# Kernel optimization log

Hardware: AMD Instinct MI355X
Metric: run time of the kernel (lower is better)

Reference implementation:

```python
import jax, jax.numpy as jnp
import numpy as np

B, S, H, G, W = 4, 4096, 1024, 256, 8
CHUNK = 1024
NUM_HEADS = 4


def _ln(x, g, b, eps=1e-5):
    m = jnp.mean(x, axis=-1, keepdims=True)
    v = jnp.var(x, axis=-1, keepdims=True)
    return (x - m) / jnp.sqrt(v + eps) * g + b


def setup_inputs() -> dict:
    key = jax.random.key(0)
    ks = jax.random.split(key, 16)
    Hm = H // 2
    return {
        "x": jax.random.normal(ks[0], (B, S, H), dtype=jnp.float32),
        # wavelet params
        "mother_wavelets": jax.random.normal(ks[1], (1, W, H, 1), dtype=jnp.float32) * 0.02,
        "scales": jnp.ones((1, W, 1, 1), dtype=jnp.float32),
        # coeff_mixer: Linear(W,H/2) -> LN -> GELU -> Linear(H/2,H)  (weights stored as (in,out))
        "mix_w1": jax.random.normal(ks[2], (W, Hm), dtype=jnp.float32) * 0.02,
        "mix_b1": jnp.zeros((Hm,), dtype=jnp.float32),
        "mix_ln_g": jnp.ones((Hm,), dtype=jnp.float32),
        "mix_ln_b": jnp.zeros((Hm,), dtype=jnp.float32),
        "mix_w2": jax.random.normal(ks[3], (Hm, H), dtype=jnp.float32) * 0.02,
        "mix_b2": jnp.zeros((H,), dtype=jnp.float32),
        # attention (no bias)
        "wq": jax.random.normal(ks[4], (H, H), dtype=jnp.float32) * 0.02,
        "wk": jax.random.normal(ks[5], (H, H), dtype=jnp.float32) * 0.02,
        "wv": jax.random.normal(ks[6], (H, H), dtype=jnp.float32) * 0.02,
        "wo": jax.random.normal(ks[7], (H, H), dtype=jnp.float32) * 0.02,
        # output_proj: LN -> Linear(H, G)
        "out_ln_g": jnp.ones((H,), dtype=jnp.float32),
        "out_ln_b": jnp.zeros((H,), dtype=jnp.float32),
        "out_w": jax.random.normal(ks[8], (H, G), dtype=jnp.float32) * 0.02,
        "out_b": jnp.zeros((G,), dtype=jnp.float32),
    }


def reference(x, mother_wavelets, scales, mix_w1, mix_b1, mix_ln_g, mix_ln_b,
              mix_w2, mix_b2, wq, wk, wv, wo, out_ln_g, out_ln_b, out_w, out_b):
    b, s, h = x.shape
    nc = s // CHUNK  # chunks are independent -> fold into batch
    xc = x.reshape(b * nc, CHUNK, h)

    # wavelet coeffs: conv1d with kernel length == channels reduces to a dot product
    norm = jnp.sqrt(jnp.sum(mother_wavelets ** 2, axis=2, keepdims=True))
    kern = (mother_wavelets / jnp.maximum(norm, 1e-12)) * jax.nn.sigmoid(scales)
    kern = kern[0, :, :, 0]  # (W, H)
    coeffs = jnp.einsum('bsh,wh->bsw', xc, kern)  # (b*nc, L, W)

    # coeff mixer
    hid = _ln(coeffs @ mix_w1 + mix_b1, mix_ln_g, mix_ln_b)
    mixed = jax.nn.gelu(hid, approximate=False) @ mix_w2 + mix_b2  # (b*nc, L, H)

    # multi-head attention within each chunk (eval mode -> no causal mask)
    hd = h // NUM_HEADS
    def heads(t):
        return t.reshape(-1, CHUNK, NUM_HEADS, hd).transpose(0, 2, 1, 3)
    q, k, v = heads(mixed @ wq), heads(mixed @ wk), heads(mixed @ wv)
    scores = jnp.einsum('bhqd,bhkd->bhqk', q, k) * (hd ** -0.5)
    attn = jax.nn.softmax(scores, axis=-1)
    o = jnp.einsum('bhqk,bhkd->bhqd', attn, v)
    o = o.transpose(0, 2, 1, 3).reshape(-1, CHUNK, h) @ wo

    # output projection with residual
    y = _ln(o + mixed, out_ln_g, out_ln_b) @ out_w + out_b  # (b*nc, L, G)
    return y.reshape(b, s, -1)
```

## Files before the change

kernel.cpp:

```cpp
#include <hip/hip_runtime.h>
#include <hip/hip_bf16.h>

typedef __bf16 bf16;
typedef __bf16 bf16x4 __attribute__((ext_vector_type(4)));
typedef __bf16 bf16x8 __attribute__((ext_vector_type(8)));
typedef float f32x4 __attribute__((ext_vector_type(4)));
typedef unsigned short ushort8_t __attribute__((ext_vector_type(8)));
typedef unsigned int u32x2 __attribute__((ext_vector_type(2)));

#define GLOAD_LDS16(g, l)                                                      \
    __builtin_amdgcn_global_load_lds(                                          \
        (const __attribute__((address_space(1))) void*)(g),                    \
        (__attribute__((address_space(3))) void*)(l), 16, 0, 0)

#define LDS_ADDR(p) ((unsigned)(uintptr_t)(__attribute__((address_space(3))) void*)(p))

#define SBAR()                                                                 \
    do {                                                                       \
        __builtin_amdgcn_sched_barrier(0);                                     \
        __builtin_amdgcn_s_barrier();                                          \
        __builtin_amdgcn_sched_barrier(0);                                     \
    } while (0)


__global__ __launch_bounds__(256) void k_wavelet(const float* __restrict__ mw,
                                                 const float* __restrict__ sc,
                                                 float* __restrict__ kern) {
    int w = blockIdx.x;
    int tid = threadIdx.x;
    float s = 0.f;
    for (int h = tid; h < 1024; h += 256) { float v = mw[w * 1024 + h]; s += v * v; }
#pragma unroll
    for (int xm = 1; xm < 64; xm <<= 1) s += __shfl_xor(s, xm);
    __shared__ float red[4];
    if ((tid & 63) == 0) red[tid >> 6] = s;
    __syncthreads();
    float tot = red[0] + red[1] + red[2] + red[3];
    float inv = 1.f / fmaxf(sqrtf(tot), 1e-12f);
    float sg = 1.f / (1.f + __expf(-sc[w]));
    float m = inv * sg;
    for (int h = tid; h < 1024; h += 256) kern[w * 1024 + h] = mw[w * 1024 + h] * m;
}

__global__ __launch_bounds__(256) void k_coeffs(const float* __restrict__ x,
                                                const float* __restrict__ kern,
                                                float* __restrict__ coeffs) {
    __shared__ float kl[8 * 1024];
    int tid = threadIdx.x;
    for (int i = tid; i < 8192; i += 256) kl[i] = kern[i];
    __syncthreads();
    int wid = tid >> 6, lane = tid & 63;
    long row = (long)blockIdx.x * 4 + wid;
    float acc[8] = {0, 0, 0, 0, 0, 0, 0, 0};
    const float* xr = x + row * 1024;
    for (int i = 0; i < 16; i++) {
        float xv = xr[lane + i * 64];
#pragma unroll
        for (int w = 0; w < 8; w++) acc[w] += xv * kl[w * 1024 + lane + i * 64];
    }
#pragma unroll
    for (int xm = 1; xm < 64; xm <<= 1) {
#pragma unroll
        for (int w = 0; w < 8; w++) acc[w] += __shfl_xor(acc[w], xm);
    }
    if (lane == 0) {
#pragma unroll
        for (int w = 0; w < 8; w++) coeffs[row * 8 + w] = acc[w];
    }
}

__global__ __launch_bounds__(256) void k_mix1(const float* __restrict__ coeffs,
                                              const float* __restrict__ w1,
                                              const float* __restrict__ b1,
                                              const float* __restrict__ lng,
                                              const float* __restrict__ lnb,
                                              bf16* __restrict__ g) {
    long row = blockIdx.x;
    int tid = threadIdx.x;
    int wid = tid >> 6, lane = tid & 63;
    __shared__ float cf[8];
    __shared__ float red1[4], red2[4];
    if (tid < 8) cf[tid] = coeffs[row * 8 + tid];
    __syncthreads();
    float h0[2];
#pragma unroll
    for (int t = 0; t < 2; t++) {
        int j = tid + t * 256;
        float a = b1[j];
#pragma unroll
        for (int w = 0; w < 8; w++) a += cf[w] * w1[w * 512 + j];
        h0[t] = a;
    }
    float s1 = h0[0] + h0[1];
    float s2 = h0[0] * h0[0] + h0[1] * h0[1];
#pragma unroll
    for (int xm = 1; xm < 64; xm <<= 1) {
        s1 += __shfl_xor(s1, xm);
        s2 += __shfl_xor(s2, xm);
    }
    if (lane == 0) { red1[wid] = s1; red2[wid] = s2; }
    __syncthreads();
    s1 = red1[0] + red1[1] + red1[2] + red1[3];
    s2 = red2[0] + red2[1] + red2[2] + red2[3];
    float mean = s1 * (1.f / 512.f);
    float var = s2 * (1.f / 512.f) - mean * mean;
    float inv = rsqrtf(var + 1e-5f);
#pragma unroll
    for (int t = 0; t < 2; t++) {
        int j = tid + t * 256;
        float xn = (h0[t] - mean) * inv * lng[j] + lnb[j];
        float ge = 0.5f * xn * (1.f + erff(xn * 0.70710678118654752f));
        g[row * 512 + j] = (bf16)ge;
    }
}

__global__ void k_wtrans_all(const float* __restrict__ w2, const float* __restrict__ wq,
                             const float* __restrict__ wk, const float* __restrict__ wv,
                             const float* __restrict__ wo, const float* __restrict__ ow,
                             bf16* __restrict__ w2t, bf16* __restrict__ wqt,
                             bf16* __restrict__ wkt, bf16* __restrict__ wvt,
                             bf16* __restrict__ wot, bf16* __restrict__ owt) {
    long idx = (long)blockIdx.x * 256 + threadIdx.x;
    if (idx < 524288) {
        int kk = (int)(idx >> 10), n = (int)(idx & 1023);
        w2t[(long)n * 512 + kk] = (bf16)w2[idx];
    } else if (idx < 4718592) {
        long r = idx - 524288;
        int m = (int)(r >> 20);
        long q = r & 1048575;
        int kk = (int)(q >> 10), n = (int)(q & 1023);
        const float* src = (m == 0) ? wq : (m == 1) ? wk : (m == 2) ? wv : wo;
        bf16* dst = (m == 0) ? wqt : (m == 1) ? wkt : (m == 2) ? wvt : wot;
        dst[(long)n * 1024 + kk] = (bf16)src[q];
    } else {
        long r = idx - 4718592;
        int kk = (int)(r >> 8), n = (int)(r & 255);
        owt[(long)n * 1024 + kk] = (bf16)ow[r];
    }
}

enum { EPI_BF16 = 0, EPI_BF16_BIAS = 1, EPI_F32_BIAS = 2, EPI_VT = 3, EPI_F32 = 4 };

template <int EPI>
__global__ __launch_bounds__(512, 2) void k_gemm8p(const bf16* __restrict__ A,
                                                   const bf16* __restrict__ Bt,
                                                   const float* __restrict__ bias,
                                                   void* __restrict__ Cout,
                                                   int K, int lda, int ldb, int ldc,
                                                   float scale) {
    __shared__ bf16 As[2 * 2 * 128 * 64];
    __shared__ bf16 Bs[2 * 2 * 128 * 64];
    const int tid = threadIdx.x;
    const int wid = tid >> 6, lane = tid & 63;
    const int wr = wid >> 2, wc = wid & 3;
    const int L = blockIdx.y * 4 + blockIdx.x;
    const int logical = ((L & 7) << 5) + (L >> 3);
    const long m0 = (long)(logical >> 2) * 256, n0 = (long)(logical & 3) * 256;
    f32x4 acc[8][4] = {};
    const int lr = lane & 15, gq = lane >> 4;
    const int l7 = lr & 7;

    const int srow = wid * 8 + (lane >> 3);
    const int sg = (lane & 7) ^ (lane >> 3);
    const bf16* aS = A + (m0 + srow) * lda + sg * 8;
    const bf16* bS = Bt + (n0 + srow) * ldb + sg * 8;

    auto stageA = [&](int t, int h) {
        bf16* d = As + (((t & 1) * 2 + h) * 128) * 64 + wid * 512;
        const long kq = (long)t << 6;
        GLOAD_LDS16(aS + (long)(h * 128) * lda + kq, d);
        GLOAD_LDS16(aS + (long)(h * 128 + 64) * lda + kq, d + 4096);
    };
    auto stageB = [&](int t, int h) {
        bf16* d = Bs + (((t & 1) * 2 + h) * 128) * 64 + wid * 512;
        const long kq = (long)t << 6;
        GLOAD_LDS16(bS + (long)(h * 128) * ldb + kq, d);
        GLOAD_LDS16(bS + (long)(h * 128 + 64) * ldb + kq, d + 4096);
    };

    bf16x8 bfr[4][2];
    auto ldB = [&](int b) {
#pragma unroll
        for (int j = 0; j < 4; j++)
#pragma unroll
            for (int kk = 0; kk < 2; kk++)
                bfr[j][kk] = *(const bf16x8*)&Bs[((b * 2 + (wc >> 1)) * 128 +
                                                 (wc & 1) * 64 + j * 16 + lr) * 64 +
                                                (((kk * 4 + gq) ^ l7) << 3)];
    };

    const int nt = K >> 6;
    const int niter = nt >> 1;

    stageA(0, 0); stageA(0, 1); stageB(0, 0); stageB(0, 1);
    stageB(1, 0); stageB(1, 1);
    asm volatile("s_waitcnt vmcnt(4)" ::: "memory");
    SBAR();

    for (int jit = 0; jit < niter - 1; ++jit) {
        const int T = jit << 1;
#pragma unroll
        for (int tp = 0; tp < 2; ++tp) {
#pragma unroll
            for (int q = 0; q < 4; ++q) {
                bf16x8 af[2][2];
                if (q == 0) ldB(tp);
#pragma unroll
                for (int ii = 0; ii < 2; ii++)
#pragma unroll
                    for (int kk = 0; kk < 2; kk++)
                        af[ii][kk] = *(const bf16x8*)&As[((tp * 2 + wr) * 128 +
                                                         (q * 2 + ii) * 16 + lr) * 64 +
                                                        (((kk * 4 + gq) ^ l7) << 3)];
                if (tp == 0) {
                    if (q == 0) stageA(T + 1, 0);
                    else if (q == 1) stageA(T + 1, 1);
                    else if (q == 2) stageB(T + 2, 0);
                    else stageB(T + 2, 1);
                } else {
                    if (q == 0) stageA(T + 2, 0);
                    else if (q == 1) stageA(T + 2, 1);
                    else if (q == 2) stageB(T + 3, 0);
                    else stageB(T + 3, 1);
                }
                if (q == 3) asm volatile("s_waitcnt vmcnt(4)" ::: "memory");
                SBAR();
                asm volatile("s_waitcnt lgkmcnt(0)" ::: "memory");
                __builtin_amdgcn_s_setprio(1);
#pragma unroll
                for (int ii = 0; ii < 2; ii++)
#pragma unroll
                    for (int j = 0; j < 4; j++) {
                        acc[q * 2 + ii][j] = __builtin_amdgcn_mfma_f32_16x16x32_bf16(
                            af[ii][0], bfr[j][0], acc[q * 2 + ii][j], 0, 0, 0);
                        acc[q * 2 + ii][j] = __builtin_amdgcn_mfma_f32_16x16x32_bf16(
                            af[ii][1], bfr[j][1], acc[q * 2 + ii][j], 0, 0, 0);
                    }
                __builtin_amdgcn_s_setprio(0);
                SBAR();
            }
        }
    }
    {
        const int T = nt - 2;
#pragma unroll
        for (int tp = 0; tp < 2; ++tp) {
#pragma unroll
            for (int q = 0; q < 4; ++q) {
                bf16x8 af[2][2];
                if (q == 0) ldB(tp);
#pragma unroll
                for (int ii = 0; ii < 2; ii++)
#pragma unroll
                    for (int kk = 0; kk < 2; kk++)
                        af[ii][kk] = *(const bf16x8*)&As[((tp * 2 + wr) * 128 +
                                                         (q * 2 + ii) * 16 + lr) * 64 +
                                                        (((kk * 4 + gq) ^ l7) << 3)];
                if (tp == 0 && q == 0) stageA(T + 1, 0);
                if (tp == 0 && q == 1) stageA(T + 1, 1);
                if (tp == 0 && q == 3) asm volatile("s_waitcnt vmcnt(0)" ::: "memory");
                SBAR();
                asm volatile("s_waitcnt lgkmcnt(0)" ::: "memory");
                __builtin_amdgcn_s_setprio(1);
#pragma unroll
                for (int ii = 0; ii < 2; ii++)
#pragma unroll
                    for (int j = 0; j < 4; j++) {
                        acc[q * 2 + ii][j] = __builtin_amdgcn_mfma_f32_16x16x32_bf16(
                            af[ii][0], bfr[j][0], acc[q * 2 + ii][j], 0, 0, 0);
                        acc[q * 2 + ii][j] = __builtin_amdgcn_mfma_f32_16x16x32_bf16(
                            af[ii][1], bfr[j][1], acc[q * 2 + ii][j], 0, 0, 0);
                    }
                __builtin_amdgcn_s_setprio(0);
                SBAR();
            }
        }
    }

    const int r0 = (lane >> 4) << 2;
#pragma unroll
    for (int i = 0; i < 8; i++) {
#pragma unroll
        for (int j = 0; j < 4; j++) {
#pragma unroll
            for (int e = 0; e < 4; e++) {
                long m = m0 + wr * 128 + i * 16 + r0 + e;
                long n = n0 + wc * 64 + j * 16 + lr;
                float v = acc[i][j][e] * scale;
                if constexpr (EPI == EPI_BF16_BIAS || EPI == EPI_F32_BIAS) v += bias[n];
                if constexpr (EPI == EPI_F32_BIAS || EPI == EPI_F32) {
                    ((float*)Cout)[m * ldc + n] = v;
                } else if constexpr (EPI == EPI_VT) {
                    long c = m >> 10, s = m & 1023, h = n >> 8, d = n & 255;
                    ((bf16*)Cout)[(((c << 2) + h) << 18) + (d << 10) + s] = (bf16)v;
                } else {
                    ((bf16*)Cout)[m * ldc + n] = (bf16)v;
                }
            }
        }
    }
}

template <int EPI>
__global__ __launch_bounds__(256) void k_gemm(const bf16* __restrict__ A,
                                              const bf16* __restrict__ Bt,
                                              const float* __restrict__ bias,
                                              void* __restrict__ Cout,
                                              int M, int N, int K,
                                              int lda, int ldb, int ldc, float scale) {
    __shared__ bf16 As[128 * 32];
    __shared__ bf16 Bs[128 * 32];
    int tid = threadIdx.x;
    int wid = tid >> 6, lane = tid & 63;
    int wr = wid >> 1, wc = wid & 1;
    const int L = blockIdx.y * 2 + blockIdx.x;
    const int logical = ((L & 7) << 5) + (L >> 3);
    long m0 = (long)(logical >> 1) * 128, n0 = (long)(logical & 1) * 128;
    f32x4 acc[4][4] = {};
    const int lr = lane & 15, ko = (lane >> 4) << 3;

    const int srow = wid * 32 + (lane >> 2);
    const int scol = (lane & 3) << 3;
    const bf16* a0 = A + (m0 + srow) * lda + scol;
    const bf16* a1 = A + (m0 + srow + 16) * lda + scol;
    const bf16* b0 = Bt + (n0 + srow) * ldb + scol;
    const bf16* b1 = Bt + (n0 + srow + 16) * ldb + scol;
    bf16* la0 = As + wid * 1024;
    bf16* la1 = As + wid * 1024 + 512;
    bf16* lb0 = Bs + wid * 1024;
    bf16* lb1 = Bs + wid * 1024 + 512;

    for (int k0 = 0; k0 < K; k0 += 32) {
        GLOAD_LDS16(a0 + k0, la0);
        GLOAD_LDS16(a1 + k0, la1);
        GLOAD_LDS16(b0 + k0, lb0);
        GLOAD_LDS16(b1 + k0, lb1);
        __syncthreads();
        bf16x8 af[4], bfr[4];
#pragma unroll
        for (int i = 0; i < 4; i++)
            af[i] = *(const bf16x8*)&As[(wr * 64 + i * 16 + lr) * 32 + ko];
#pragma unroll
        for (int i = 0; i < 4; i++)
            bfr[i] = *(const bf16x8*)&Bs[(wc * 64 + i * 16 + lr) * 32 + ko];
#pragma unroll
        for (int i = 0; i < 4; i++) {
#pragma unroll
            for (int j = 0; j < 4; j++)
                acc[i][j] = __builtin_amdgcn_mfma_f32_16x16x32_bf16(af[i], bfr[j], acc[i][j], 0, 0, 0);
        }
        __syncthreads();
    }
    const int r0 = (lane >> 4) << 2;
#pragma unroll
    for (int i = 0; i < 4; i++) {
#pragma unroll
        for (int j = 0; j < 4; j++) {
#pragma unroll
            for (int e = 0; e < 4; e++) {
                long m = m0 + wr * 64 + i * 16 + r0 + e;
                long n = n0 + wc * 64 + j * 16 + lr;
                float v = acc[i][j][e] * scale;
                if constexpr (EPI == EPI_BF16_BIAS || EPI == EPI_F32_BIAS) v += bias[n];
                if constexpr (EPI == EPI_F32_BIAS || EPI == EPI_F32) {
                    ((float*)Cout)[m * ldc + n] = v;
                } else {
                    ((bf16*)Cout)[m * ldc + n] = (bf16)v;
                }
            }
        }
    }
}

__global__ __launch_bounds__(512, 2) void k_attn(const bf16* __restrict__ q,
                                                 const bf16* __restrict__ k,
                                                 const bf16* __restrict__ vt,
                                                 bf16* __restrict__ ao) {
    __shared__ __align__(16) bf16 smem[2 * 16384 + 2 * 16384 + 8192];
    bf16* Ks = smem;
    bf16* Vs = smem + 32768;
    bf16* Ps = smem + 65536;
    int tid = threadIdx.x;
    int wid = tid >> 6, lane = tid & 63;
    int c = blockIdx.x, h = blockIdx.y, q0 = blockIdx.z * 128;
    const int lr = lane & 15, gq = lane >> 4, ko = gq << 3;
    const int l7 = lr & 7;

    const int krw = wid * 2 + (lane >> 5);
    const int kg = (lane & 31) ^ (krw & 7);
    const bf16* ksrc = k + ((long)c << 10) * 1024 + h * 256 + kg * 8;
    const int vrw = wid * 8 + ((lane >> 3) & 7);
    const int vg = (lane & 7) ^ ((lane >> 3) & 7);
    const bf16* vsrc = vt + ((long)(c * 4 + h) << 18) + vg * 8;

    long qrow = ((long)c << 10) + q0 + wid * 16 + lr;
    bf16x8 qf[8];
#pragma unroll
    for (int kk = 0; kk < 8; kk++)
        qf[kk] = *(const bf16x8*)&q[qrow * 1024 + h * 256 + kk * 32 + ko];

    f32x4 oacc[16] = {};
    float m_run[4] = {-1e30f, -1e30f, -1e30f, -1e30f};
    float l_run[4] = {0.f, 0.f, 0.f, 0.f};

    bf16* PT = Ps + (wid << 10);
    const unsigned pva = LDS_ADDR(&PT[(gq << 7) + lr]);

#pragma unroll
    for (int i = 0; i < 4; i++) {
        GLOAD_LDS16(ksrc + (long)(i * 16 + krw) * 1024, Ks + i * 4096 + wid * 512);
        GLOAD_LDS16(vsrc + (long)(i * 64 + vrw) * 1024, Vs + i * 4096 + wid * 512);
    }
    __syncthreads();
    int buf = 0;
    for (int t = 0; t < 16; t++) {
        if (t < 15) {
            const int kb = (t + 1) << 6;
            const int ob = (buf ^ 1) << 14;
#pragma unroll
            for (int i = 0; i < 4; i++) {
                GLOAD_LDS16(ksrc + (long)(kb + i * 16 + krw) * 1024, Ks + ob + i * 4096 + wid * 512);
                GLOAD_LDS16(vsrc + (long)(i * 64 + vrw) * 1024 + kb, Vs + ob + i * 4096 + wid * 512);
            }
        }
        const bf16* Kc = Ks + (buf << 14);
        const bf16* Vc = Vs + (buf << 14);
        f32x4 s[4] = {};
        __builtin_amdgcn_s_setprio(1);
#pragma unroll
        for (int kk = 0; kk < 8; kk++) {
#pragma unroll
            for (int n = 0; n < 4; n++)
                s[n] = __builtin_amdgcn_mfma_f32_16x16x32_bf16(
                    qf[kk],
                    *(const bf16x8*)&Kc[((n * 16 + lr) << 8) + ((((kk << 2) + gq) ^ l7) << 3)],
                    s[n], 0, 0, 0);
        }
        __builtin_amdgcn_s_setprio(0);
        float mx[4];
#pragma unroll
        for (int e = 0; e < 4; e++)
            mx[e] = fmaxf(fmaxf(s[0][e], s[1][e]), fmaxf(s[2][e], s[3][e]));
#pragma unroll
        for (int xm = 1; xm < 16; xm <<= 1) {
#pragma unroll
            for (int e = 0; e < 4; e++) mx[e] = fmaxf(mx[e], __shfl_xor(mx[e], xm));
        }
        bool need = (mx[0] > m_run[0] + 8.f) || (mx[1] > m_run[1] + 8.f) ||
                    (mx[2] > m_run[2] + 8.f) || (mx[3] > m_run[3] + 8.f);
        if (__any(need)) {
#pragma unroll
            for (int e = 0; e < 4; e++) {
                float mn = fmaxf(m_run[e], mx[e]);
                float al = __expf(m_run[e] - mn);
                m_run[e] = mn;
                l_run[e] *= al;
#pragma unroll
                for (int f = 0; f < 16; f++) oacc[f][e] *= al;
            }
        }
        float rs[4] = {0.f, 0.f, 0.f, 0.f};
#pragma unroll
        for (int n = 0; n < 4; n++) {
#pragma unroll
            for (int e = 0; e < 4; e++) {
                float p = __expf(s[n][e] - m_run[e]);
                s[n][e] = p;
                rs[e] += p;
            }
        }
#pragma unroll
        for (int xm = 1; xm < 16; xm <<= 1) {
#pragma unroll
            for (int e = 0; e < 4; e++) rs[e] += __shfl_xor(rs[e], xm);
        }
#pragma unroll
        for (int e = 0; e < 4; e++) l_run[e] += rs[e];
#pragma unroll
        for (int n = 0; n < 4; n++) {
            bf16x4 pv = {(bf16)s[n][0], (bf16)s[n][1], (bf16)s[n][2], (bf16)s[n][3]};
            *(bf16x4*)&PT[((n * 16 + lr) << 4) + (gq << 2)] = pv;
        }
        asm volatile("s_waitcnt lgkmcnt(0)" ::: "memory");
        u32x2 t0, t1, t2, t3;
        asm volatile("ds_read_b64_tr_b16 %0, %1" : "=v"(t0) : "v"(pva));
        asm volatile("ds_read_b64_tr_b16 %0, %1 offset:128" : "=v"(t1) : "v"(pva));
        asm volatile("ds_read_b64_tr_b16 %0, %1 offset:1024" : "=v"(t2) : "v"(pva));
        asm volatile("ds_read_b64_tr_b16 %0, %1 offset:1152" : "=v"(t3) : "v"(pva));
        asm volatile("s_waitcnt lgkmcnt(0)" ::: "memory");
        __builtin_amdgcn_sched_barrier(0);
        union { u32x2 u[2]; bf16x8 v; } p0, p1;
        p0.u[0] = t0; p0.u[1] = t1;
        p1.u[0] = t2; p1.u[1] = t3;
        const bf16x8 pf0 = p0.v, pf1 = p1.v;
        __builtin_amdgcn_s_setprio(1);
#pragma unroll
        for (int n2 = 0; n2 < 16; n2++) {
            const int vrow = (n2 * 16 + lr) << 6;
            const int vswz = gq ^ l7;
            oacc[n2] = __builtin_amdgcn_mfma_f32_16x16x32_bf16(
                pf0, *(const bf16x8*)&Vc[vrow + (vswz << 3)], oacc[n2], 0, 0, 0);
            oacc[n2] = __builtin_amdgcn_mfma_f32_16x16x32_bf16(
                pf1, *(const bf16x8*)&Vc[vrow + ((vswz ^ 4) << 3)], oacc[n2], 0, 0, 0);
        }
        __builtin_amdgcn_s_setprio(0);
        __syncthreads();
        buf ^= 1;
    }
#pragma unroll
    for (int n2 = 0; n2 < 16; n2++) {
#pragma unroll
        for (int e = 0; e < 4; e++) {
            long row = ((long)c << 10) + q0 + wid * 16 + (gq << 2) + e;
            long col = ((long)h << 8) + n2 * 16 + lr;
            ao[row * 1024 + col] = (bf16)(oacc[n2][e] / l_run[e]);
        }
    }
}

__global__ __launch_bounds__(256) void k_outln(const bf16* __restrict__ o,
                                               const bf16* __restrict__ mixed,
                                               const float* __restrict__ g,
                                               const float* __restrict__ b,
                                               bf16* __restrict__ t) {
    long row = blockIdx.x;
    int tid = threadIdx.x;
    int wid = tid >> 6, lane = tid & 63;
    __shared__ float red1[4], red2[4];
    float x[4];
    const bf16* orow = o + row * 1024;
    const bf16* mrow = mixed + row * 1024;
    bf16x4 ov = *(const bf16x4*)&orow[tid * 4];
    bf16x4 mv = *(const bf16x4*)&mrow[tid * 4];
#pragma unroll
    for (int i = 0; i < 4; i++) x[i] = (float)ov[i] + (float)mv[i];
    float s1 = x[0] + x[1] + x[2] + x[3];
    float s2 = x[0] * x[0] + x[1] * x[1] + x[2] * x[2] + x[3] * x[3];
#pragma unroll
    for (int xm = 1; xm < 64; xm <<= 1) {
        s1 += __shfl_xor(s1, xm);
        s2 += __shfl_xor(s2, xm);
    }
    if (lane == 0) { red1[wid] = s1; red2[wid] = s2; }
    __syncthreads();
    s1 = red1[0] + red1[1] + red1[2] + red1[3];
    s2 = red2[0] + red2[1] + red2[2] + red2[3];
    float mean = s1 * (1.f / 1024.f);
    float var = s2 * (1.f / 1024.f) - mean * mean;
    float inv = rsqrtf(var + 1e-5f);
#pragma unroll
    for (int i = 0; i < 4; i++) {
        int j = tid * 4 + i;
        t[row * 1024 + j] = (bf16)((x[i] - mean) * inv * g[j] + b[j]);
    }
}

extern "C" void kernel_launch(void* const* d_in, const int* in_sizes, int n_in,
                              void* d_out, int out_size, void* d_ws, size_t ws_size,
                              hipStream_t stream) {
    const float* x   = (const float*)d_in[0];
    const float* mw  = (const float*)d_in[1];
    const float* sc  = (const float*)d_in[2];
    const float* w1  = (const float*)d_in[3];
    const float* b1  = (const float*)d_in[4];
    const float* lng1 = (const float*)d_in[5];
    const float* lnb1 = (const float*)d_in[6];
    const float* w2  = (const float*)d_in[7];
    const float* b2  = (const float*)d_in[8];
    const float* wq  = (const float*)d_in[9];
    const float* wk  = (const float*)d_in[10];
    const float* wv  = (const float*)d_in[11];
    const float* wo  = (const float*)d_in[12];
    const float* lng2 = (const float*)d_in[13];
    const float* lnb2 = (const float*)d_in[14];
    const float* ow  = (const float*)d_in[15];
    const float* ob  = (const float*)d_in[16];

    char* p = (char*)d_ws;
    auto take = [&](size_t bytes) {
        char* r = p;
        p += (bytes + 255) & ~(size_t)255;
        return r;
    };
    const size_t M = 16384;
    float* kern   = (float*)take(8 * 1024 * sizeof(float));
    float* coeffs = (float*)take(M * 8 * sizeof(float));
    bf16* g       = (bf16*)take(M * 512 * 2);
    bf16* mixed   = (bf16*)take(M * 1024 * 2);
    bf16* qb      = (bf16*)take(M * 1024 * 2 * 2);
    bf16* kb2     = qb + M * 1024;
    bf16* obf     = qb;
    bf16* vtb     = (bf16*)take(M * 1024 * 2);
    bf16* tb      = vtb;
    bf16* aob     = (bf16*)take(M * 1024 * 2);
    bf16* w2t     = (bf16*)take((size_t)1024 * 512 * 2);
    bf16* wqt     = (bf16*)take((size_t)1024 * 1024 * 2);
    bf16* wkt     = (bf16*)take((size_t)1024 * 1024 * 2);
    bf16* wvt     = (bf16*)take((size_t)1024 * 1024 * 2);
    bf16* wot     = (bf16*)take((size_t)1024 * 1024 * 2);
    bf16* owt     = (bf16*)take((size_t)256 * 1024 * 2);

    k_wavelet<<<8, 256, 0, stream>>>(mw, sc, kern);
    k_coeffs<<<4096, 256, 0, stream>>>(x, kern, coeffs);
    k_mix1<<<16384, 256, 0, stream>>>(coeffs, w1, b1, lng1, lnb1, g);

    k_wtrans_all<<<19456, 256, 0, stream>>>(w2, wq, wk, wv, wo, ow,
                                            w2t, wqt, wkt, wvt, wot, owt);

    k_gemm8p<EPI_BF16_BIAS><<<dim3(4, 64), 512, 0, stream>>>(
        g, w2t, b2, mixed, 512, 512, 512, 1024, 1.f);
    k_gemm8p<EPI_BF16><<<dim3(4, 64), 512, 0, stream>>>(
        mixed, wqt, nullptr, qb, 1024, 1024, 1024, 1024, 0.0625f);
    k_gemm8p<EPI_BF16><<<dim3(4, 64), 512, 0, stream>>>(
        mixed, wkt, nullptr, kb2, 1024, 1024, 1024, 1024, 1.f);
    k_gemm8p<EPI_VT><<<dim3(4, 64), 512, 0, stream>>>(
        mixed, wvt, nullptr, vtb, 1024, 1024, 1024, 1024, 1.f);
    k_attn<<<dim3(16, 4, 8), 512, 0, stream>>>(qb, kb2, vtb, aob);
    k_gemm8p<EPI_BF16><<<dim3(4, 64), 512, 0, stream>>>(
        aob, wot, nullptr, obf, 1024, 1024, 1024, 1024, 1.f);
    k_outln<<<16384, 256, 0, stream>>>(obf, mixed, lng2, lnb2, tb);
    k_gemm<EPI_F32_BIAS><<<dim3(2, 128), 256, 0, stream>>>(
        tb, owt, ob, d_out, 16384, 256, 1024, 1024, 1024, 256, 1.f);
}
```

Baseline: 414.0 us.

## Compute transposed scores so P feeds PV MFMA from registers without LDS

```diff
diff --git a/kernel.cpp b/kernel.cpp
--- a/kernel.cpp
+++ b/kernel.cpp
@@ -12,8 +12,6 @@
     __builtin_amdgcn_global_load_lds(                                          \
         (const __attribute__((address_space(1))) void*)(g),                    \
         (__attribute__((address_space(3))) void*)(l), 16, 0, 0)
-
-#define LDS_ADDR(p) ((unsigned)(uintptr_t)(__attribute__((address_space(3))) void*)(p))
 
 #define SBAR()                                                                 \
     do {                                                                       \
@@ -376,10 +374,9 @@
                                                  const bf16* __restrict__ k,
                                                  const bf16* __restrict__ vt,
                                                  bf16* __restrict__ ao) {
-    __shared__ __align__(16) bf16 smem[2 * 16384 + 2 * 16384 + 8192];
+    __shared__ __align__(16) bf16 smem[2 * 16384 + 2 * 16384];
     bf16* Ks = smem;
     bf16* Vs = smem + 32768;
-    bf16* Ps = smem + 65536;
     int tid = threadIdx.x;
     int wid = tid >> 6, lane = tid & 63;
     int c = blockIdx.x, h = blockIdx.y, q0 = blockIdx.z * 128;
@@ -400,11 +397,13 @@
         qf[kk] = *(const bf16x8*)&q[qrow * 1024 + h * 256 + kk * 32 + ko];
 
     f32x4 oacc[16] = {};
-    float m_run[4] = {-1e30f, -1e30f, -1e30f, -1e30f};
-    float l_run[4] = {0.f, 0.f, 0.f, 0.f};
-
-    bf16* PT = Ps + (wid << 10);
-    const unsigned pva = LDS_ADDR(&PT[(gq << 7) + lr]);
+    float m_run = -1e30f, l_run = 0.f;
+
+    const int vco[4] = {
+        (((gq >> 1) ^ l7) << 3) + ((gq & 1) << 2),
+        (((2 + (gq >> 1)) ^ l7) << 3) + ((gq & 1) << 2),
+        (((4 + (gq >> 1)) ^ l7) << 3) + ((gq & 1) << 2),
+        (((6 + (gq >> 1)) ^ l7) << 3) + ((gq & 1) << 2)};
 
 #pragma unroll
     for (int i = 0; i < 4; i++) {
@@ -425,95 +424,94 @@
         }
         const bf16* Kc = Ks + (buf << 14);
         const bf16* Vc = Vs + (buf << 14);
-        f32x4 s[4] = {};
+        f32x4 st[4] = {};
         __builtin_amdgcn_s_setprio(1);
 #pragma unroll
         for (int kk = 0; kk < 8; kk++) {
 #pragma unroll
             for (int n = 0; n < 4; n++)
-                s[n] = __builtin_amdgcn_mfma_f32_16x16x32_bf16(
-                    qf[kk],
+                st[n] = __builtin_amdgcn_mfma_f32_16x16x32_bf16(
                     *(const bf16x8*)&Kc[((n * 16 + lr) << 8) + ((((kk << 2) + gq) ^ l7) << 3)],
-                    s[n], 0, 0, 0);
+                    qf[kk], st[n], 0, 0, 0);
         }
         __builtin_amdgcn_s_setprio(0);
-        float mx[4];
-#pragma unroll
-        for (int e = 0; e < 4; e++)
-            mx[e] = fmaxf(fmaxf(s[0][e], s[1][e]), fmaxf(s[2][e], s[3][e]));
-#pragma unroll
-        for (int xm = 1; xm < 16; xm <<= 1) {
-#pragma unroll
-            for (int e = 0; e < 4; e++) mx[e] = fmaxf(mx[e], __shfl_xor(mx[e], xm));
-        }
-        bool need = (mx[0] > m_run[0] + 8.f) || (mx[1] > m_run[1] + 8.f) ||
-                    (mx[2] > m_run[2] + 8.f) || (mx[3] > m_run[3] + 8.f);
-        if (__any(need)) {
+        float mx = st[0][0];
+#pragma unroll
+        for (int n = 0; n < 4; n++)
+#pragma unroll
+            for (int e = 0; e < 4; e++) mx = fmaxf(mx, st[n][e]);
+        mx = fmaxf(mx, __shfl_xor(mx, 16));
+        mx = fmaxf(mx, __shfl_xor(mx, 32));
+        if (__any(mx > m_run + 8.f)) {
+            float mn = fmaxf(m_run, mx);
+            float al = __expf(m_run - mn);
+            m_run = mn;
+            l_run *= al;
+            float alx[4];
+#pragma unroll
+            for (int e = 0; e < 4; e++) alx[e] = __shfl(al, (gq << 2) + e);
+#pragma unroll
+            for (int f = 0; f < 16; f++)
+#pragma unroll
+                for (int e = 0; e < 4; e++) oacc[f][e] *= alx[e];
+        }
+        float rs = 0.f;
+#pragma unroll
+        for (int n = 0; n < 4; n++)
 #pragma unroll
             for (int e = 0; e < 4; e++) {
-                float mn = fmaxf(m_run[e], mx[e]);
-                float al = __expf(m_run[e] - mn);
-                m_run[e] = mn;
-                l_run[e] *= al;
-#pragma unroll
-                for (int f = 0; f < 16; f++) oacc[f][e] *= al;
+                float p = __expf(st[n][e] - m_run);
+                st[n][e] = p;
+                rs += p;
             }
-        }
-        float rs[4] = {0.f, 0.f, 0.f, 0.f};
-#pragma unroll
-        for (int n = 0; n < 4; n++) {
+        rs += __shfl_xor(rs, 16);
+        rs += __shfl_xor(rs, 32);
+        l_run += rs;
+        bf16x4 pa0, pa1, pa2, pa3;
+#pragma unroll
+        for (int e = 0; e < 4; e++) {
+            pa0[e] = (bf16)st[0][e];
+            pa1[e] = (bf16)st[1][e];
+            pa2[e] = (bf16)st[2][e];
+            pa3[e] = (bf16)st[3][e];
+        }
+        bf16x8 af0, af1;
+#pragma unroll
+        for (int e = 0; e < 4; e++) {
+            af0[e] = pa0[e]; af0[e + 4] = pa1[e];
+            af1[e] = pa2[e]; af1[e + 4] = pa3[e];
+        }
+        __builtin_amdgcn_s_setprio(1);
+#pragma unroll
+        for (int n2 = 0; n2 < 16; n2++) {
+            const int rowoff = (n2 * 16 + lr) << 6;
+            bf16x4 v00 = *(const bf16x4*)&Vc[rowoff + vco[0]];
+            bf16x4 v01 = *(const bf16x4*)&Vc[rowoff + vco[1]];
+            bf16x4 v10 = *(const bf16x4*)&Vc[rowoff + vco[2]];
+            bf16x4 v11 = *(const bf16x4*)&Vc[rowoff + vco[3]];
+            bf16x8 vb0, vb1;
 #pragma unroll
             for (int e = 0; e < 4; e++) {
-                float p = __expf(s[n][e] - m_run[e]);
-                s[n][e] = p;
-                rs[e] += p;
+                vb0[e] = v00[e]; vb0[e + 4] = v01[e];
+                vb1[e] = v10[e]; vb1[e + 4] = v11[e];
             }
-        }
-#pragma unroll
-        for (int xm = 1; xm < 16; xm <<= 1) {
-#pragma unroll
-            for (int e = 0; e < 4; e++) rs[e] += __shfl_xor(rs[e], xm);
-        }
-#pragma unroll
-        for (int e = 0; e < 4; e++) l_run[e] += rs[e];
-#pragma unroll
-        for (int n = 0; n < 4; n++) {
-            bf16x4 pv = {(bf16)s[n][0], (bf16)s[n][1], (bf16)s[n][2], (bf16)s[n][3]};
-            *(bf16x4*)&PT[((n * 16 + lr) << 4) + (gq << 2)] = pv;
-        }
-        asm volatile("s_waitcnt lgkmcnt(0)" ::: "memory");
-        u32x2 t0, t1, t2, t3;
-        asm volatile("ds_read_b64_tr_b16 %0, %1" : "=v"(t0) : "v"(pva));
-        asm volatile("ds_read_b64_tr_b16 %0, %1 offset:128" : "=v"(t1) : "v"(pva));
-        asm volatile("ds_read_b64_tr_b16 %0, %1 offset:1024" : "=v"(t2) : "v"(pva));
-        asm volatile("ds_read_b64_tr_b16 %0, %1 offset:1152" : "=v"(t3) : "v"(pva));
-        asm volatile("s_waitcnt lgkmcnt(0)" ::: "memory");
-        __builtin_amdgcn_sched_barrier(0);
-        union { u32x2 u[2]; bf16x8 v; } p0, p1;
-        p0.u[0] = t0; p0.u[1] = t1;
-        p1.u[0] = t2; p1.u[1] = t3;
-        const bf16x8 pf0 = p0.v, pf1 = p1.v;
-        __builtin_amdgcn_s_setprio(1);
-#pragma unroll
-        for (int n2 = 0; n2 < 16; n2++) {
-            const int vrow = (n2 * 16 + lr) << 6;
-            const int vswz = gq ^ l7;
-            oacc[n2] = __builtin_amdgcn_mfma_f32_16x16x32_bf16(
-                pf0, *(const bf16x8*)&Vc[vrow + (vswz << 3)], oacc[n2], 0, 0, 0);
-            oacc[n2] = __builtin_amdgcn_mfma_f32_16x16x32_bf16(
-                pf1, *(const bf16x8*)&Vc[vrow + ((vswz ^ 4) << 3)], oacc[n2], 0, 0, 0);
+            oacc[n2] = __builtin_amdgcn_mfma_f32_16x16x32_bf16(af0, vb0, oacc[n2], 0, 0, 0);
+            oacc[n2] = __builtin_amdgcn_mfma_f32_16x16x32_bf16(af1, vb1, oacc[n2], 0, 0, 0);
         }
         __builtin_amdgcn_s_setprio(0);
         __syncthreads();
         buf ^= 1;
     }
+    float ldiv[4];
+#pragma unroll
+    for (int e = 0; e < 4; e++) ldiv[e] = 1.f / __shfl(l_run, (gq << 2) + e);
 #pragma unroll
     for (int n2 = 0; n2 < 16; n2++) {
 #pragma unroll
         for (int e = 0; e < 4; e++) {
             long row = ((long)c << 10) + q0 + wid * 16 + (gq << 2) + e;
             long col = ((long)h << 8) + n2 * 16 + lr;
-            ao[row * 1024 + col] = (bf16)(oacc[n2][e] / l_run[e]);
+            ao[row * 1024 + col] = (bf16)(oacc[n2][e] * ldiv[e]);
         }
     }
 }
```

Result: no change. 420.7 us (+1.6%).

## Fuse wavelet coeffs with mixer LN/GELU and tile weight transposes via LDS

Applied to the files above, without the earlier changes.

```diff
diff --git a/kernel.cpp b/kernel.cpp
--- a/kernel.cpp
+++ b/kernel.cpp
@@ -42,9 +42,13 @@
     for (int h = tid; h < 1024; h += 256) kern[w * 1024 + h] = mw[w * 1024 + h] * m;
 }
 
-__global__ __launch_bounds__(256) void k_coeffs(const float* __restrict__ x,
-                                                const float* __restrict__ kern,
-                                                float* __restrict__ coeffs) {
+__global__ __launch_bounds__(256) void k_front(const float* __restrict__ x,
+                                               const float* __restrict__ kern,
+                                               const float* __restrict__ w1,
+                                               const float* __restrict__ b1,
+                                               const float* __restrict__ lng,
+                                               const float* __restrict__ lnb,
+                                               bf16* __restrict__ g) {
     __shared__ float kl[8 * 1024];
     int tid = threadIdx.x;
     for (int i = tid; i < 8192; i += 256) kl[i] = kern[i];
@@ -63,79 +67,70 @@
 #pragma unroll
         for (int w = 0; w < 8; w++) acc[w] += __shfl_xor(acc[w], xm);
     }
-    if (lane == 0) {
-#pragma unroll
-        for (int w = 0; w < 8; w++) coeffs[row * 8 + w] = acc[w];
-    }
-}
-
-__global__ __launch_bounds__(256) void k_mix1(const float* __restrict__ coeffs,
-                                              const float* __restrict__ w1,
-                                              const float* __restrict__ b1,
-                                              const float* __restrict__ lng,
-                                              const float* __restrict__ lnb,
-                                              bf16* __restrict__ g) {
-    long row = blockIdx.x;
-    int tid = threadIdx.x;
-    int wid = tid >> 6, lane = tid & 63;
-    __shared__ float cf[8];
-    __shared__ float red1[4], red2[4];
-    if (tid < 8) cf[tid] = coeffs[row * 8 + tid];
-    __syncthreads();
-    float h0[2];
-#pragma unroll
-    for (int t = 0; t < 2; t++) {
-        int j = tid + t * 256;
+    float h[8];
+#pragma unroll
+    for (int e = 0; e < 8; e++) {
+        int j = lane * 8 + e;
         float a = b1[j];
 #pragma unroll
-        for (int w = 0; w < 8; w++) a += cf[w] * w1[w * 512 + j];
-        h0[t] = a;
-    }
-    float s1 = h0[0] + h0[1];
-    float s2 = h0[0] * h0[0] + h0[1] * h0[1];
+        for (int w = 0; w < 8; w++) a += acc[w] * w1[w * 512 + j];
+        h[e] = a;
+    }
+    float s1 = 0.f, s2 = 0.f;
+#pragma unroll
+    for (int e = 0; e < 8; e++) { s1 += h[e]; s2 += h[e] * h[e]; }
 #pragma unroll
     for (int xm = 1; xm < 64; xm <<= 1) {
         s1 += __shfl_xor(s1, xm);
         s2 += __shfl_xor(s2, xm);
     }
-    if (lane == 0) { red1[wid] = s1; red2[wid] = s2; }
-    __syncthreads();
-    s1 = red1[0] + red1[1] + red1[2] + red1[3];
-    s2 = red2[0] + red2[1] + red2[2] + red2[3];
     float mean = s1 * (1.f / 512.f);
     float var = s2 * (1.f / 512.f) - mean * mean;
     float inv = rsqrtf(var + 1e-5f);
-#pragma unroll
-    for (int t = 0; t < 2; t++) {
-        int j = tid + t * 256;
-        float xn = (h0[t] - mean) * inv * lng[j] + lnb[j];
+    bf16x8 out;
+#pragma unroll
+    for (int e = 0; e < 8; e++) {
+        int j = lane * 8 + e;
+        float xn = (h[e] - mean) * inv * lng[j] + lnb[j];
         float ge = 0.5f * xn * (1.f + erff(xn * 0.70710678118654752f));
-        g[row * 512 + j] = (bf16)ge;
-    }
-}
-
-__global__ void k_wtrans_all(const float* __restrict__ w2, const float* __restrict__ wq,
-                             const float* __restrict__ wk, const float* __restrict__ wv,
-                             const float* __restrict__ wo, const float* __restrict__ ow,
-                             bf16* __restrict__ w2t, bf16* __restrict__ wqt,
-                             bf16* __restrict__ wkt, bf16* __restrict__ wvt,
-                             bf16* __restrict__ wot, bf16* __restrict__ owt) {
-    long idx = (long)blockIdx.x * 256 + threadIdx.x;
-    if (idx < 524288) {
-        int kk = (int)(idx >> 10), n = (int)(idx & 1023);
-        w2t[(long)n * 512 + kk] = (bf16)w2[idx];
-    } else if (idx < 4718592) {
-        long r = idx - 524288;
-        int m = (int)(r >> 20);
-        long q = r & 1048575;
-        int kk = (int)(q >> 10), n = (int)(q & 1023);
-        const float* src = (m == 0) ? wq : (m == 1) ? wk : (m == 2) ? wv : wo;
-        bf16* dst = (m == 0) ? wqt : (m == 1) ? wkt : (m == 2) ? wvt : wot;
-        dst[(long)n * 1024 + kk] = (bf16)src[q];
-    } else {
-        long r = idx - 4718592;
-        int kk = (int)(r >> 8), n = (int)(r & 255);
-        owt[(long)n * 1024 + kk] = (bf16)ow[r];
+        out[e] = (bf16)ge;
+    }
+    *(bf16x8*)&g[row * 512 + lane * 8] = out;
+}
+
+__global__ __launch_bounds__(256) void k_wtrans_t(const float* __restrict__ w2, const float* __restrict__ wq,
+                                                  const float* __restrict__ wk, const float* __restrict__ wv,
+                                                  const float* __restrict__ wo, const float* __restrict__ ow,
+                                                  bf16* __restrict__ w2t, bf16* __restrict__ wqt,
+                                                  bf16* __restrict__ wkt, bf16* __restrict__ wvt,
+                                                  bf16* __restrict__ wot, bf16* __restrict__ owt) {
+    __shared__ float ld[32][33];
+    const int t = blockIdx.x;
+    const int tid = threadIdx.x;
+    const float* src;
+    bf16* dst;
+    int K, N, lt;
+    if (t < 512)       { src = w2; dst = w2t; K = 512;  N = 1024; lt = t; }
+    else if (t < 1536) { src = wq; dst = wqt; K = 1024; N = 1024; lt = t - 512; }
+    else if (t < 2560) { src = wk; dst = wkt; K = 1024; N = 1024; lt = t - 1536; }
+    else if (t < 3584) { src = wv; dst = wvt; K = 1024; N = 1024; lt = t - 2560; }
+    else if (t < 4608) { src = wo; dst = wot; K = 1024; N = 1024; lt = t - 3584; }
+    else               { src = ow; dst = owt; K = 1024; N = 256;  lt = t - 4608; }
+    int kt, nt_;
+    if (t < 4608) { kt = lt >> 5; nt_ = lt & 31; }
+    else          { kt = lt >> 3; nt_ = lt & 7; }
+    const int k0 = kt << 5, n0 = nt_ << 5;
+    const int tx = tid & 31, ty = tid >> 5;
+#pragma unroll
+    for (int m = 0; m < 4; m++) {
+        int r = ty + m * 8;
+        ld[r][tx] = src[(long)(k0 + r) * N + n0 + tx];
+    }
+    __syncthreads();
+#pragma unroll
+    for (int m = 0; m < 4; m++) {
+        int r = ty + m * 8;
+        dst[(long)(n0 + r) * K + k0 + tx] = (bf16)ld[tx][r];
     }
 }
 
@@ -584,7 +579,6 @@
     };
     const size_t M = 16384;
     float* kern   = (float*)take(8 * 1024 * sizeof(float));
-    float* coeffs = (float*)take(M * 8 * sizeof(float));
     bf16* g       = (bf16*)take(M * 512 * 2);
     bf16* mixed   = (bf16*)take(M * 1024 * 2);
     bf16* qb      = (bf16*)take(M * 1024 * 2 * 2);
@@ -601,11 +595,10 @@
     bf16* owt     = (bf16*)take((size_t)256 * 1024 * 2);
 
     k_wavelet<<<8, 256, 0, stream>>>(mw, sc, kern);
-    k_coeffs<<<4096, 256, 0, stream>>>(x, kern, coeffs);
-    k_mix1<<<16384, 256, 0, stream>>>(coeffs, w1, b1, lng1, lnb1, g);
-
-    k_wtrans_all<<<19456, 256, 0, stream>>>(w2, wq, wk, wv, wo, ow,
-                                            w2t, wqt, wkt, wvt, wot, owt);
+    k_front<<<4096, 256, 0, stream>>>(x, kern, w1, b1, lng1, lnb1, g);
+
+    k_wtrans_t<<<4864, 256, 0, stream>>>(w2, wq, wk, wv, wo, ow,
+                                         w2t, wqt, wkt, wvt, wot, owt);
 
     k_gemm8p<EPI_BF16_BIAS><<<dim3(4, 64), 512, 0, stream>>>(
         g, w2t, b2, mixed, 512, 512, 512, 1024, 1.f);
```

Measured after the change: 408.1 us, median of 2. No clear change (-1.4%).
